# Kernel optimization log

Measured on AMD Instinct MI355X. Metric: run time of the kernel, lower is better.

Reference implementation:

```python
import jax, jax.numpy as jnp
import numpy as np

N, T, C, H, W = 16, 8, 256, 14, 14
IC = 64          # inter_channels
SCALE = 32       # nearest-upsample factor (scale_s); scale_t = 1


def setup_inputs() -> dict:
    key = jax.random.key(0)
    kx, kq1, kq2, kv1, kl, ki = jax.random.split(key, 6)
    cin = C + 1
    x = jax.random.normal(kx, (N, T, C, H, W), dtype=jnp.float32)
    lam = jax.random.uniform(kl, (), dtype=jnp.float32)
    index = jax.random.randint(ki, (N,), 0, N)
    # nn.Linear default init: U(-1/sqrt(fan_in), 1/sqrt(fan_in))
    bound = 1.0 / np.sqrt(cin)
    Wq = jax.random.uniform(kq1, (IC, cin), minval=-bound, maxval=bound, dtype=jnp.float32)
    bq = jax.random.uniform(kq2, (IC,), minval=-bound, maxval=bound, dtype=jnp.float32)
    Wv = jax.random.uniform(kv1, (1, cin), minval=-bound, maxval=bound, dtype=jnp.float32)
    Wv = Wv.at[0, C].set(4.0)   # value.weight.data[0, in_channel] = 4
    bv = jnp.zeros((1,), dtype=jnp.float32)  # value.bias.data[:] = 0
    return {"x": x, "lam": lam, "index": index, "Wq": Wq, "bq": bq, "Wv": Wv, "bv": bv}


def reference(x, lam, index, Wq, bq, Wv, bv):
    n, t, c, h, w = x.shape
    ic = Wq.shape[0]
    nt, hw = n * t, h * w
    x_lam = x.reshape(nt, c, h, w)
    x_lam_ = x[index].reshape(nt, c, h, w)           # batch-shuffled partner
    lam_block = jnp.broadcast_to(lam - 0.5, (nt, 1, h, w)).astype(x.dtype)
    x_lam = jnp.concatenate([x_lam, lam_block], axis=1)     # [nt, c+1, h, w]
    x_lam_ = jnp.concatenate([x_lam_, -lam_block], axis=1)
    # linear over channel dim (equivalent to the transpose(1,3)/Linear/transpose dance)
    q = jnp.einsum('nchw,dc->ndhw', x_lam, Wq) + bq[None, :, None, None]
    k = jnp.einsum('nchw,dc->ndhw', x_lam_, Wq) + bq[None, :, None, None]
    v = jnp.einsum('nchw,dc->ndhw', x_lam_, Wv) + bv[None, :, None, None]
    q_x = q.reshape(nt, ic, hw).transpose(0, 2, 1)   # [nt, hw, ic]
    k_x = k.reshape(nt, ic, hw)                      # [nt, ic, hw]
    v_ = v.reshape(nt, 1, hw).transpose(0, 2, 1)     # [nt, hw, 1]
    scores = jnp.einsum('nqd,ndk->nqk', q_x, k_x) / jnp.sqrt(jnp.float32(ic))
    attn = jax.nn.softmax(scores, axis=-1)           # [nt, hw, hw]
    mask_lam_ = jnp.matmul(attn.astype(jnp.float32), v_.astype(jnp.float32))
    mask_lam_ = mask_lam_.reshape(nt, 1, h, w)       # scale_t == 1 so expand is a no-op
    # F.interpolate(mode='nearest', scale_factor=SCALE)
    mask_lam_ = jnp.repeat(jnp.repeat(mask_lam_, SCALE, axis=2), SCALE, axis=3)
    mask_lam_ = jax.nn.sigmoid(mask_lam_)
    mask = jnp.concatenate([1.0 - mask_lam_, mask_lam_], axis=1)  # [nt, 2, h*S, w*S]
    v_out = v_.reshape(n, t, h, w)                    # (n, t*scale_t, h, w)
    return mask, v_out
```

## Files before the change

### kernel.cpp

```cpp
#include <hip/hip_runtime.h>
#include <hip/hip_bf16.h>
#include <stdint.h>

#define HWsz 196
#define NTs  128
#define MASK_ELEMS 51380224
#define VOUT_OFF   MASK_ELEMS
#define MASK_CHUNKS 6422528

#define WLAM_OFF 8192
#define BQ_OFF   8256
#define WV_OFF   8320
#define LAM_OFF  8577
#define BV_OFF   8578
#define XT_OFF_F 8704
#define EQ_OFF_F 3221504
#define EK_OFF_F 4024704
#define V_OFF    4827904
#define SIG_OFF  4852992

typedef __attribute__((ext_vector_type(8))) short short8;
typedef __attribute__((ext_vector_type(4))) float f32x4;

__device__ __forceinline__ bool is_bf16_mode(const void* wv) {
  return ((const uint16_t*)wv)[256] == (uint16_t)0x4080;
}

__device__ __forceinline__ float ldf(const void* p, int i, bool bf) {
  if (bf) {
    uint32_t u = (uint32_t)((const uint16_t*)p)[i] << 16;
    return __builtin_bit_cast(float, u);
  }
  return ((const float*)p)[i];
}

__device__ __forceinline__ uint16_t f2bf(float f) {
  __hip_bfloat16 h = __float2bfloat16(f);
  return __builtin_bit_cast(uint16_t, h);
}

__device__ __forceinline__ float bf2f(uint16_t u) {
  uint32_t v = (uint32_t)u << 16;
  return __builtin_bit_cast(float, v);
}

__global__ __launch_bounds__(256) void k0_prep(const void* Wq, const void* bq,
                                               const void* Wv, const void* lam,
                                               const void* bv, float* ws) {
  int idx = blockIdx.x * 256 + threadIdx.x;
  bool bf = is_bf16_mode(Wv);
  if (idx < 16384) {
    int d = idx >> 8, c = idx & 255;
    ((uint16_t*)ws)[idx] = f2bf(ldf(Wq, d * 257 + c, bf));
  } else if (idx < 16448) {
    int d = idx - 16384;
    ws[WLAM_OFF + d] = ldf(Wq, d * 257 + 256, bf);
  } else if (idx < 16512) {
    ws[BQ_OFF + idx - 16448] = ldf(bq, idx - 16448, bf);
  } else if (idx < 16769) {
    ws[WV_OFF + idx - 16512] = ldf(Wv, idx - 16512, bf);
  } else if (idx == 16769) {
    ws[LAM_OFF] = ldf(lam, 0, bf) - 0.5f;
  } else if (idx == 16770) {
    ws[BV_OFF] = ldf(bv, 0, bf);
  }
}

__global__ __launch_bounds__(256) void k_xt(const void* xraw, const void* Wvraw, float* ws) {
  __shared__ uint16_t lds[64 * 196];
  bool bf = is_bf16_mode(Wvraw);
  int s = blockIdx.x >> 2, ch = blockIdx.x & 3;
  size_t base = ((size_t)s * 256 + ch * 64) * 196;
  if (bf) {
    const uint4* src = (const uint4*)((const uint16_t*)xraw + base);
    uint4* dst = (uint4*)lds;
    for (int i = threadIdx.x; i < 1568; i += 256) dst[i] = src[i];
  } else {
    const float* src = (const float*)xraw + base;
    for (int i = threadIdx.x; i < 12544; i += 256) lds[i] = f2bf(src[i]);
  }
  __syncthreads();
  uint32_t* xt = (uint32_t*)((uint16_t*)(ws + XT_OFF_F));
  for (int i = threadIdx.x; i < 6272; i += 256) {
    int j = i >> 5, cc2 = i & 31;
    uint32_t lo = lds[(cc2 * 2) * 196 + j];
    uint32_t hi = lds[(cc2 * 2 + 1) * 196 + j];
    xt[((size_t)s * 196 + j) * 128 + ch * 32 + cc2] = lo | (hi << 16);
  }
}

__global__ __launch_bounds__(256) void k1_qk(const int* index, const void* Wvraw,
                                             float* ws, void* dout) {
  int b = blockIdx.x;
  int isK = (b >= NTs) ? 1 : 0;
  int s = isK ? b - NTs : b;
  int t = s & 7;
  int src = isK ? index[s >> 3] * 8 + t : s;
  bool outbf = is_bf16_mode(Wvraw);
  const uint16_t* xTs = (const uint16_t*)(ws + XT_OFF_F) + (size_t)src * 196 * 256;
  const uint16_t* wqb = (const uint16_t*)ws;
  int lane = threadIdx.x & 63, w = threadIdx.x >> 6;
  int ln = lane & 15, quad = lane >> 4;

  f32x4 acc[13];
#pragma unroll
  for (int mt = 0; mt < 13; mt++) acc[mt] = (f32x4){0.f, 0.f, 0.f, 0.f};

#pragma unroll
  for (int kc = 0; kc < 8; kc++) {
    short8 bfrag = *(const short8*)(wqb + ((w * 16 + ln) * 256 + kc * 32 + quad * 8));
#pragma unroll
    for (int mt = 0; mt < 13; mt++) {
      short8 afrag = *(const short8*)(xTs + ((mt * 16 + ln) * 256 + kc * 32 + quad * 8));
      acc[mt] = __builtin_amdgcn_mfma_f32_16x16x32_bf16(afrag, bfrag, acc[mt], 0, 0, 0);
    }
  }

  float lamv = ws[LAM_OFF];
  float lamch = isK ? -lamv : lamv;
  int d = w * 16 + ln;
  float addend = ws[WLAM_OFF + d] * lamch + ws[BQ_OFF + d];
  uint16_t* E = (uint16_t*)(ws + (isK ? EK_OFF_F : EQ_OFF_F));
#pragma unroll
  for (int mt = 0; mt < 13; mt++) {
#pragma unroll
    for (int r = 0; r < 4; r++) {
      int j = mt * 16 + quad * 4 + r;
      if (j < 196) E[((size_t)s * 196 + j) * 64 + d] = f2bf(acc[mt][r] + addend);
    }
  }

  if (isK && threadIdx.x < 196) {
    int j = threadIdx.x;
    float vacc = 0.f;
    const uint16_t* xr = xTs + j * 256;
    for (int c0 = 0; c0 < 256; c0 += 8) {
      short8 xv = *(const short8*)(xr + c0);
#pragma unroll
      for (int i = 0; i < 8; i++)
        vacc = fmaf(bf2f((uint16_t)xv[i]), ws[WV_OFF + c0 + i], vacc);
    }
    float vvv = vacc + ws[WV_OFF + 256] * lamch + ws[BV_OFF];
    ws[V_OFF + s * HWsz + j] = vvv;
    if (outbf) ((uint16_t*)dout)[VOUT_OFF + s * HWsz + j] = f2bf(vvv);
    else       ((float*)dout)[VOUT_OFF + s * HWsz + j] = vvv;
  }
}

__global__ __launch_bounds__(256) void k2_attn(float* ws) {
  int s = blockIdx.x >> 2, blk = blockIdx.x & 3;
  int lane = threadIdx.x & 63, w = threadIdx.x >> 6;
  int mt = blk * 4 + w;
  if (mt >= 13) return;
  int ln = lane & 15, quad = lane >> 4;
  const uint16_t* Eq = (const uint16_t*)(ws + EQ_OFF_F);
  const uint16_t* Ek = (const uint16_t*)(ws + EK_OFF_F);

  const uint16_t* qrow = Eq + ((size_t)s * 196 + mt * 16 + ln) * 64 + quad * 8;
  short8 aq0 = *(const short8*)(qrow);
  short8 aq1 = *(const short8*)(qrow + 32);

  float vcol[13];
  f32x4 acc[13];
#pragma unroll
  for (int nt = 0; nt < 13; nt++) {
    int col = nt * 16 + ln;
    vcol[nt] = (col < 196) ? ws[V_OFF + s * 196 + col] : 0.f;
    const uint16_t* krow = Ek + ((size_t)s * 196 + col) * 64 + quad * 8;
    short8 b0 = *(const short8*)(krow);
    short8 b1 = *(const short8*)(krow + 32);
    f32x4 a = (f32x4){0.f, 0.f, 0.f, 0.f};
    a = __builtin_amdgcn_mfma_f32_16x16x32_bf16(aq0, b0, a, 0, 0, 0);
    a = __builtin_amdgcn_mfma_f32_16x16x32_bf16(aq1, b1, a, 0, 0, 0);
    acc[nt] = a;
  }

  float mx[4] = {-1e30f, -1e30f, -1e30f, -1e30f};
#pragma unroll
  for (int nt = 0; nt < 13; nt++) {
    bool valid = (nt * 16 + ln) < 196;
#pragma unroll
    for (int r = 0; r < 4; r++) {
      float sv = valid ? acc[nt][r] * 0.125f : -1e30f;
      acc[nt][r] = sv;
      mx[r] = fmaxf(mx[r], sv);
    }
  }
#pragma unroll
  for (int m = 1; m < 16; m <<= 1)
#pragma unroll
    for (int r = 0; r < 4; r++) mx[r] = fmaxf(mx[r], __shfl_xor(mx[r], m));

  float l[4] = {0.f, 0.f, 0.f, 0.f}, av[4] = {0.f, 0.f, 0.f, 0.f};
#pragma unroll
  for (int nt = 0; nt < 13; nt++)
#pragma unroll
    for (int r = 0; r < 4; r++) {
      float p = __expf(acc[nt][r] - mx[r]);
      l[r] += p;
      av[r] += p * vcol[nt];
    }
#pragma unroll
  for (int m = 1; m < 16; m <<= 1)
#pragma unroll
    for (int r = 0; r < 4; r++) {
      l[r] += __shfl_xor(l[r], m);
      av[r] += __shfl_xor(av[r], m);
    }

  if (ln == 0) {
#pragma unroll
    for (int r = 0; r < 4; r++) {
      int j = mt * 16 + quad * 4 + r;
      if (j < 196) {
        float mval = av[r] / l[r];
        ws[SIG_OFF + s * 196 + j] = 1.f / (1.f + __expf(-mval));
      }
    }
  }
}

__global__ __launch_bounds__(256) void k3_mask(const float* ws, void* dout, const void* Wvraw) {
  bool bf = is_bf16_mode(Wvraw);
  int stride = gridDim.x * 256;
  for (int idx = blockIdx.x * 256 + threadIdx.x; idx < MASK_CHUNKS; idx += stride) {
    int c8  = idx % 56;
    int row = idx / 56;
    int y   = row % 448;
    int tmp = row / 448;
    float m = ws[SIG_OFF + (tmp >> 1) * HWsz + (y >> 5) * 14 + (c8 >> 2)];
    float val = (tmp & 1) ? m : 1.0f - m;
    if (bf) {
      uint32_t ub = (uint32_t)f2bf(val);
      uint32_t pk = ub | (ub << 16);
      uint4 qv; qv.x = pk; qv.y = pk; qv.z = pk; qv.w = pk;
      ((uint4*)dout)[idx] = qv;
    } else {
      float4 f = make_float4(val, val, val, val);
      ((float4*)dout)[(size_t)idx * 2]     = f;
      ((float4*)dout)[(size_t)idx * 2 + 1] = f;
    }
  }
}

extern "C" void kernel_launch(void* const* d_in, const int* in_sizes, int n_in,
                              void* d_out, int out_size, void* d_ws, size_t ws_size,
                              hipStream_t stream) {
  const void* x   = d_in[0];
  const void* lam = d_in[1];
  const int* idx  = (const int*)d_in[2];
  const void* Wq  = d_in[3];
  const void* bq  = d_in[4];
  const void* Wv  = d_in[5];
  const void* bv  = d_in[6];
  float* ws = (float*)d_ws;

  k0_prep<<<66, 256, 0, stream>>>(Wq, bq, Wv, lam, bv, ws);
  k_xt<<<512, 256, 0, stream>>>(x, Wv, ws);
  k1_qk<<<256, 256, 0, stream>>>(idx, Wv, ws, d_out);
  k2_attn<<<512, 256, 0, stream>>>(ws);
  k3_mask<<<6272, 256, 0, stream>>>(ws, d_out, Wv);
}
```

Measured before the change: 277.0 us.

## Fuse x transpose into QK projection kernel via swizzled LDS staging

Removes the separate k_xt kernel, which wrote a transposed bf16 copy of x to workspace. k1_qk now loads raw x in 64-channel chunks into LDS, transposes them into an XOR-swizzled layout, and feeds the MFMA from LDS. The V projection is also computed from the staged chunk. This saves a kernel launch and a global round trip for x. In exchange, K blocks re-read and re-convert x, and the grid is only 256 blocks with extra syncs per chunk.

```diff
diff --git a/kernel.cpp b/kernel.cpp
--- a/kernel.cpp
+++ b/kernel.cpp
@@ -13,7 +13,6 @@
 #define WV_OFF   8320
 #define LAM_OFF  8577
 #define BV_OFF   8578
-#define XT_OFF_F 8704
 #define EQ_OFF_F 3221504
 #define EK_OFF_F 4024704
 #define V_OFF    4827904
@@ -66,53 +65,77 @@
   }
 }
 
-__global__ __launch_bounds__(256) void k_xt(const void* xraw, const void* Wvraw, float* ws) {
-  __shared__ uint16_t lds[64 * 196];
-  bool bf = is_bf16_mode(Wvraw);
-  int s = blockIdx.x >> 2, ch = blockIdx.x & 3;
-  size_t base = ((size_t)s * 256 + ch * 64) * 196;
-  if (bf) {
-    const uint4* src = (const uint4*)((const uint16_t*)xraw + base);
-    uint4* dst = (uint4*)lds;
-    for (int i = threadIdx.x; i < 1568; i += 256) dst[i] = src[i];
-  } else {
-    const float* src = (const float*)xraw + base;
-    for (int i = threadIdx.x; i < 12544; i += 256) lds[i] = f2bf(src[i]);
-  }
-  __syncthreads();
-  uint32_t* xt = (uint32_t*)((uint16_t*)(ws + XT_OFF_F));
-  for (int i = threadIdx.x; i < 6272; i += 256) {
-    int j = i >> 5, cc2 = i & 31;
-    uint32_t lo = lds[(cc2 * 2) * 196 + j];
-    uint32_t hi = lds[(cc2 * 2 + 1) * 196 + j];
-    xt[((size_t)s * 196 + j) * 128 + ch * 32 + cc2] = lo | (hi << 16);
-  }
-}
-
-__global__ __launch_bounds__(256) void k1_qk(const int* index, const void* Wvraw,
-                                             float* ws, void* dout) {
+__global__ __launch_bounds__(256) void k1_qk(const void* xraw, const int* index,
+                                             const void* Wvraw, float* ws, void* dout) {
+  __shared__ __align__(16) uint16_t Abuf[64 * 200];
+  __shared__ __align__(16) uint16_t Bbuf[208 * 64];
   int b = blockIdx.x;
   int isK = (b >= NTs) ? 1 : 0;
   int s = isK ? b - NTs : b;
   int t = s & 7;
   int src = isK ? index[s >> 3] * 8 + t : s;
-  bool outbf = is_bf16_mode(Wvraw);
-  const uint16_t* xTs = (const uint16_t*)(ws + XT_OFF_F) + (size_t)src * 196 * 256;
+  bool bf = is_bf16_mode(Wvraw);
+  int tid = threadIdx.x;
+  int lane = tid & 63, w = tid >> 6;
+  int ln = lane & 15, quad = lane >> 4;
+
   const uint16_t* wqb = (const uint16_t*)ws;
-  int lane = threadIdx.x & 63, w = threadIdx.x >> 6;
-  int ln = lane & 15, quad = lane >> 4;
+  size_t xbase = (size_t)src * 256 * 196;
 
   f32x4 acc[13];
 #pragma unroll
   for (int mt = 0; mt < 13; mt++) acc[mt] = (f32x4){0.f, 0.f, 0.f, 0.f};
-
-#pragma unroll
-  for (int kc = 0; kc < 8; kc++) {
-    short8 bfrag = *(const short8*)(wqb + ((w * 16 + ln) * 256 + kc * 32 + quad * 8));
-#pragma unroll
-    for (int mt = 0; mt < 13; mt++) {
-      short8 afrag = *(const short8*)(xTs + ((mt * 16 + ln) * 256 + kc * 32 + quad * 8));
-      acc[mt] = __builtin_amdgcn_mfma_f32_16x16x32_bf16(afrag, bfrag, acc[mt], 0, 0, 0);
+  float vacc = 0.f;
+
+#pragma unroll 1
+  for (int chunk = 0; chunk < 4; chunk++) {
+    __syncthreads();
+    if (bf) {
+      for (int i2 = tid; i2 < 3136; i2 += 256) {
+        int c = i2 / 49, jj = i2 - c * 49;
+        uint2 val = *(const uint2*)((const uint16_t*)xraw + xbase +
+                                    (size_t)(chunk * 64 + c) * 196 + jj * 4);
+        *(uint2*)(Abuf + c * 200 + jj * 4) = val;
+      }
+    } else {
+      for (int i2 = tid; i2 < 3136; i2 += 256) {
+        int c = i2 / 49, jj = i2 - c * 49;
+        float4 v4 = *(const float4*)((const float*)xraw + xbase +
+                                     (size_t)(chunk * 64 + c) * 196 + jj * 4);
+        uint2 pk;
+        pk.x = (uint32_t)f2bf(v4.x) | ((uint32_t)f2bf(v4.y) << 16);
+        pk.y = (uint32_t)f2bf(v4.z) | ((uint32_t)f2bf(v4.w) << 16);
+        *(uint2*)(Abuf + c * 200 + jj * 4) = pk;
+      }
+    }
+    __syncthreads();
+    for (int i = tid; i < 6272; i += 256) {
+      int c2 = i / 196, j = i - c2 * 196;
+      uint32_t lo = Abuf[(2 * c2) * 200 + j];
+      uint32_t hi = Abuf[(2 * c2 + 1) * 200 + j];
+      int g  = c2 >> 2;
+      int gp = g ^ (j & 7);
+      ((uint32_t*)Bbuf)[j * 32 + gp * 4 + (c2 & 3)] = lo | (hi << 16);
+    }
+    __syncthreads();
+#pragma unroll
+    for (int kc2 = 0; kc2 < 2; kc2++) {
+      short8 bfrag = *(const short8*)(wqb + (size_t)(w * 16 + ln) * 256 +
+                                      chunk * 64 + kc2 * 32 + quad * 8);
+      int gp = (kc2 * 4 + quad) ^ (ln & 7);
+#pragma unroll
+      for (int mt = 0; mt < 13; mt++) {
+        int j = mt * 16 + ln;
+        short8 afrag = *(const short8*)(Bbuf + j * 64 + ((kc2 * 4 + quad) ^ (j & 7)) * 8);
+        (void)gp;
+        acc[mt] = __builtin_amdgcn_mfma_f32_16x16x32_bf16(afrag, bfrag, acc[mt], 0, 0, 0);
+      }
+    }
+    if (isK && tid < HWsz) {
+      const float* wvp = ws + WV_OFF + chunk * 64;
+#pragma unroll 4
+      for (int c = 0; c < 64; c++)
+        vacc = fmaf(bf2f(Abuf[c * 200 + tid]), wvp[c], vacc);
     }
   }
 
@@ -126,24 +149,16 @@
 #pragma unroll
     for (int r = 0; r < 4; r++) {
       int j = mt * 16 + quad * 4 + r;
-      if (j < 196) E[((size_t)s * 196 + j) * 64 + d] = f2bf(acc[mt][r] + addend);
-    }
-  }
-
-  if (isK && threadIdx.x < 196) {
-    int j = threadIdx.x;
-    float vacc = 0.f;
-    const uint16_t* xr = xTs + j * 256;
-    for (int c0 = 0; c0 < 256; c0 += 8) {
-      short8 xv = *(const short8*)(xr + c0);
-#pragma unroll
-      for (int i = 0; i < 8; i++)
-        vacc = fmaf(bf2f((uint16_t)xv[i]), ws[WV_OFF + c0 + i], vacc);
-    }
+      if (j < HWsz) E[((size_t)s * HWsz + j) * 64 + d] = f2bf(acc[mt][r] + addend);
+    }
+  }
+
+  if (isK && tid < HWsz) {
     float vvv = vacc + ws[WV_OFF + 256] * lamch + ws[BV_OFF];
-    ws[V_OFF + s * HWsz + j] = vvv;
-    if (outbf) ((uint16_t*)dout)[VOUT_OFF + s * HWsz + j] = f2bf(vvv);
-    else       ((float*)dout)[VOUT_OFF + s * HWsz + j] = vvv;
+    ws[V_OFF + s * HWsz + tid] = vvv;
+    bool outbf = bf;
+    if (outbf) ((uint16_t*)dout)[VOUT_OFF + s * HWsz + tid] = f2bf(vvv);
+    else       ((float*)dout)[VOUT_OFF + s * HWsz + tid] = vvv;
   }
 }
 
@@ -256,8 +271,7 @@
   float* ws = (float*)d_ws;
 
   k0_prep<<<66, 256, 0, stream>>>(Wq, bq, Wv, lam, bv, ws);
-  k_xt<<<512, 256, 0, stream>>>(x, Wv, ws);
-  k1_qk<<<256, 256, 0, stream>>>(idx, Wv, ws, d_out);
+  k1_qk<<<256, 256, 0, stream>>>(x, idx, Wv, ws, d_out);
   k2_attn<<<512, 256, 0, stream>>>(ws);
   k3_mask<<<6272, 256, 0, stream>>>(ws, d_out, Wv);
 }
```

New measurement: 275.1 us. No clear change (-0.7%).
